# Optimization experiments

Measured on AMD Instinct MI355X. Metric: run time of the kernel, lower is better.

Reference implementation:

```python
import jax, jax.numpy as jnp
import numpy as np

N = 100_000      # nodes
E = 3_200_000    # edges (avg degree 32)
DIM = 512        # input feature dim
HID = 16         # GCNConv hidden dim (fixed in __init__)
C = 64           # n_classes
DROP_P = 0.5     # F.dropout default


def _gcn_conv(x, W, b, row, col, deg_inv_sqrt, n_nodes):
    """PyG GCNConv: h = x@W; out[j] += norm_ij * h[i]; out += b.
    row/col already include self-loops; deg_inv_sqrt precomputed."""
    h = x @ W                                  # [N, out]
    norm = deg_inv_sqrt[row] * deg_inv_sqrt[col]  # [E+N]
    msg = h[row] * norm[:, None]               # gather + scale
    out = jax.ops.segment_sum(msg, col, num_segments=n_nodes)
    return out + b


def setup_inputs() -> dict:
    key = jax.random.key(0)
    k = jax.random.split(key, 6)
    x = jax.random.normal(k[0], (N, DIM), dtype=jnp.float32)
    edge_index = jax.random.randint(k[1], (2, E), 0, N, dtype=jnp.int32)
    W1 = jax.random.normal(k[2], (DIM, HID), dtype=jnp.float32) * (1.0 / np.sqrt(DIM))
    b1 = jnp.zeros((HID,), dtype=jnp.float32)
    W2 = jax.random.normal(k[3], (HID, C), dtype=jnp.float32) * (1.0 / np.sqrt(HID))
    b2 = jnp.zeros((C,), dtype=jnp.float32)
    return {"x": x, "edge_index": edge_index, "W1": W1, "b1": b1, "W2": W2, "b2": b2}


def reference(x, edge_index, W1, b1, W2, b2):
    n = x.shape[0]
    loops = jnp.arange(n, dtype=edge_index.dtype)
    row = jnp.concatenate([edge_index[0], loops])  # sources (with self-loops)
    col = jnp.concatenate([edge_index[1], loops])  # targets (with self-loops)
    # symmetric normalization: deg over targets with unit edge weight
    deg = jax.ops.segment_sum(jnp.ones_like(col, dtype=x.dtype), col, num_segments=n)
    deg_inv_sqrt = jnp.where(deg > 0, jax.lax.rsqrt(deg), 0.0)

    h = jax.nn.relu(_gcn_conv(x, W1, b1, row, col, deg_inv_sqrt, n))
    # F.dropout(x) -> p=0.5, training=True; deterministic fixed key
    keep = jax.random.bernoulli(jax.random.key(42), 1.0 - DROP_P, h.shape)
    h = jnp.where(keep, h / (1.0 - DROP_P), 0.0)
    logits = _gcn_conv(h, W2, b2, row, col, deg_inv_sqrt, n)
    return jax.nn.log_softmax(logits, axis=1)
```

## Files before the change

kernel.cpp:

```cpp
#include <hip/hip_runtime.h>

#define NN    100000
#define NE    3200000
#define DIMK  512
#define HIDN  16
#define NCLS  64
#define NBUCK 391
#define NBLK  512
#define CHUNK 6250
#define BCAP  10240

__device__ __forceinline__ unsigned rotl32(unsigned x, int r){ return (x << r) | (x >> (32 - r)); }

__device__ __forceinline__ unsigned threefry_bits(unsigned i){
  const unsigned k0 = 0u, k1 = 42u;
  const unsigned k2 = 0x1BD11BDAu ^ k0 ^ k1;
  unsigned a = 0u + k0, b = i + k1;
#define TF_R(r) { a += b; b = rotl32(b, (r)); b ^= a; }
  TF_R(13) TF_R(15) TF_R(26) TF_R(6)  a += k1; b += k2 + 1u;
  TF_R(17) TF_R(29) TF_R(16) TF_R(24) a += k2; b += k0 + 2u;
  TF_R(13) TF_R(15) TF_R(26) TF_R(6)  a += k0; b += k1 + 3u;
  TF_R(17) TF_R(29) TF_R(16) TF_R(24) a += k1; b += k2 + 4u;
  TF_R(13) TF_R(15) TF_R(26) TF_R(6)  a += k2; b += k0 + 5u;
#undef TF_R
  return a ^ b;
}

__global__ __launch_bounds__(256) void kp1_hist(const int* __restrict__ col, int* __restrict__ M){
  __shared__ int h[NBUCK];
  const int blk = blockIdx.x, t = threadIdx.x;
  for (int q = t; q < NBUCK; q += 256) h[q] = 0;
  __syncthreads();
  const int e0 = blk * CHUNK;
  for (int i = t; i < CHUNK; i += 256)
    atomicAdd(&h[col[e0 + i] >> 8], 1);
  __syncthreads();
  for (int q = t; q < NBUCK; q += 256) M[blk * NBUCK + q] = h[q];
}

__global__ __launch_bounds__(512) void kp2_rowscan(int* __restrict__ M, int* __restrict__ btot){
  __shared__ int s[512];
  const int b = blockIdx.x, t = threadIdx.x;
  const int idx = t * NBUCK + b;
  int v = M[idx];
  int x = v;
  s[t] = x; __syncthreads();
  for (int d = 1; d < 512; d <<= 1){
    int y = (t >= d) ? s[t - d] : 0;
    __syncthreads();
    x += y; s[t] = x;
    __syncthreads();
  }
  M[idx] = x - v;
  if (t == 511) btot[b] = x;
}

__global__ __launch_bounds__(512) void kp2b_bscan(const int* __restrict__ btot, int* __restrict__ bbase){
  __shared__ int s[512];
  const int t = threadIdx.x;
  int v = (t < NBUCK) ? btot[t] : 0;
  int x = v;
  s[t] = x; __syncthreads();
  for (int d = 1; d < 512; d <<= 1){
    int y = (t >= d) ? s[t - d] : 0;
    __syncthreads();
    x += y; s[t] = x;
    __syncthreads();
  }
  if (t < NBUCK) bbase[t] = x - v;
  if (t == NBUCK - 1) bbase[NBUCK] = x;
}

__global__ __launch_bounds__(256) void kp3_scatter(const int* __restrict__ row, const int* __restrict__ col,
                                                   const int* __restrict__ M, const int* __restrict__ bbase,
                                                   unsigned* __restrict__ coarse){
  __shared__ int cur[NBUCK];
  const int blk = blockIdx.x, t = threadIdx.x;
  for (int q = t; q < NBUCK; q += 256) cur[q] = bbase[q] + M[blk * NBUCK + q];
  __syncthreads();
  const int e0 = blk * CHUNK;
  for (int i = t; i < CHUNK; i += 256){
    int c = col[e0 + i];
    int r = row[e0 + i];
    int p = atomicAdd(&cur[c >> 8], 1);
    coarse[p] = ((unsigned)(c & 255) << 17) | (unsigned)r;
  }
}

__global__ __launch_bounds__(1024) void kd_meta(const unsigned* __restrict__ coarse,
                                                const int* __restrict__ bbase,
                                                int* __restrict__ dstart,
                                                int* __restrict__ dcnt,
                                                float* __restrict__ dis){
  __shared__ int cnt[256], s[256];
  const int b = blockIdx.x, t = threadIdx.x;
  if (t < 256) cnt[t] = 0;
  __syncthreads();
  const int base = bbase[b];
  const int nreg = bbase[b + 1] - base;
  for (int i = t; i < nreg; i += 1024)
    atomicAdd(&cnt[coarse[base + i] >> 17], 1);
  __syncthreads();
  int deg = 0, x = 0;
  if (t < 256){ deg = cnt[t]; x = deg; s[t] = x; }
  __syncthreads();
  for (int d = 1; d < 256; d <<= 1){
    int y = 0;
    if (t < 256 && t >= d) y = s[t - d];
    __syncthreads();
    if (t < 256){ x += y; s[t] = x; }
    __syncthreads();
  }
  if (t < 256){
    int n = (b << 8) + t;
    if (n < NN){
      dstart[n] = base + (x - deg);
      dcnt[n]   = deg;
      dis[n]    = rsqrtf((float)(deg + 1));
    }
  }
}

__global__ __launch_bounds__(256) void k_gemm1(const float* __restrict__ x,
                                               const float* __restrict__ W1,
                                               const float* __restrict__ dis,
                                               _Float16* __restrict__ hs16){
  const int lane = threadIdx.x & 63;
  const int wid  = (blockIdx.x * blockDim.x + threadIdx.x) >> 6;
  const int nw   = (gridDim.x * blockDim.x) >> 6;
  const bool s5 = (lane & 32) != 0;
  const bool s4 = (lane & 16) != 0;
  const bool s3 = (lane & 8)  != 0;
  const bool s2 = (lane & 4)  != 0;

  float4 w4[8][4];
  const float4* W1v = (const float4*)W1;
#pragma unroll
  for (int k = 0; k < 8; ++k)
#pragma unroll
    for (int jj = 0; jj < 4; ++jj)
      w4[k][jj] = W1v[(lane * 8 + k) * 4 + jj];

  for (int n = wid; n < NN; n += nw){
    const float4* xp = (const float4*)(x + (size_t)n * DIMK + lane * 8);
    float4 xa = xp[0], xb = xp[1];
    float xv[8] = {xa.x, xa.y, xa.z, xa.w, xb.x, xb.y, xb.z, xb.w};
    float acc[16];
#pragma unroll
    for (int j = 0; j < 16; ++j) acc[j] = 0.f;
#pragma unroll
    for (int k = 0; k < 8; ++k){
      float xk = xv[k];
#pragma unroll
      for (int jj = 0; jj < 4; ++jj){
        acc[jj*4+0] = fmaf(xk, w4[k][jj].x, acc[jj*4+0]);
        acc[jj*4+1] = fmaf(xk, w4[k][jj].y, acc[jj*4+1]);
        acc[jj*4+2] = fmaf(xk, w4[k][jj].z, acc[jj*4+2]);
        acc[jj*4+3] = fmaf(xk, w4[k][jj].w, acc[jj*4+3]);
      }
    }
    float t8[8];
#pragma unroll
    for (int m = 0; m < 8; ++m){
      float keep = s5 ? acc[8+m] : acc[m];
      float give = s5 ? acc[m]   : acc[8+m];
      t8[m] = keep + __shfl_xor(give, 32, 64);
    }
    float t4[4];
#pragma unroll
    for (int m = 0; m < 4; ++m){
      float keep = s4 ? t8[4+m] : t8[m];
      float give = s4 ? t8[m]   : t8[4+m];
      t4[m] = keep + __shfl_xor(give, 16, 64);
    }
    float t2[2];
#pragma unroll
    for (int m = 0; m < 2; ++m){
      float keep = s3 ? t4[2+m] : t4[m];
      float give = s3 ? t4[m]   : t4[2+m];
      t2[m] = keep + __shfl_xor(give, 8, 64);
    }
    float keep = s2 ? t2[1] : t2[0];
    float give = s2 ? t2[0] : t2[1];
    float v = keep + __shfl_xor(give, 4, 64);
    v += __shfl_xor(v, 2, 64);
    v += __shfl_xor(v, 1, 64);
    float hv = __shfl(v, (lane & 15) * 4, 64);
    if (lane < 16) hs16[(size_t)n * HIDN + lane] = (_Float16)(hv * dis[n]);
  }
}

__global__ __launch_bounds__(1024) void k_sortagg1(const unsigned* __restrict__ coarse,
                                                   const int* __restrict__ bbase,
                                                   const int* __restrict__ dstart,
                                                   const int* __restrict__ dcnt,
                                                   const _Float16* __restrict__ hs16,
                                                   const float* __restrict__ dis,
                                                   const float* __restrict__ b1,
                                                   _Float16* __restrict__ h2s16){
  __shared__ int ldsCsr[BCAP];
  __shared__ int ofs[256], cnt[256], rk[256];
  const int b = blockIdx.x, t = threadIdx.x;
  const int base = bbase[b];
  const int nreg = min(bbase[b + 1] - base, BCAP);
  if (t < 256){
    int n = (b << 8) + t;
    rk[t] = 0;
    if (n < NN){ ofs[t] = dstart[n] - base; cnt[t] = dcnt[n]; }
    else       { ofs[t] = 0;               cnt[t] = 0; }
  }
  __syncthreads();
  for (int i = t; i < nreg; i += 1024){
    unsigned p = coarse[base + i];
    int l = p >> 17;
    int q = atomicAdd(&rk[l], 1);
    ldsCsr[ofs[l] + q] = (int)(p & 0x1FFFFu);
  }
  __syncthreads();
  const int g = t >> 4, j = t & 15;
  for (int d = g; d < 256; d += 64){
    const int n = (b << 8) + d;
    if (n >= NN) break;
    const int st = ofs[d], cn = cnt[d];
    float acc = 0.f;
    int i = 0;
    for (; i + 2 <= cn; i += 2){
      int r0 = ldsCsr[st + i];
      int r1 = ldsCsr[st + i + 1];
      float a0 = (float)hs16[r0 * HIDN + j];
      float a1 = (float)hs16[r1 * HIDN + j];
      acc += a0 + a1;
    }
    if (i < cn) acc += (float)hs16[ldsCsr[st + i] * HIDN + j];
    float dn = dis[n];
    float v = fmaf(dn, acc + (float)hs16[(size_t)n * HIDN + j], b1[j]);
    v = fmaxf(v, 0.f);
    unsigned bits = threefry_bits((unsigned)(n * HIDN + j));
    float kept = (bits & 0x80000000u) ? 0.f : v * 2.f;
    h2s16[(size_t)n * HIDN + j] = (_Float16)(kept * dn);
  }
}

__global__ __launch_bounds__(1024) void k_agg2b(const unsigned* __restrict__ coarse,
                                                const int* __restrict__ bbase,
                                                const int* __restrict__ dstart,
                                                const int* __restrict__ dcnt,
                                                const _Float16* __restrict__ h2s16,
                                                const float* __restrict__ dis,
                                                const float* __restrict__ W2,
                                                const float* __restrict__ b2,
                                                float* __restrict__ out){
  __shared__ int ldsCsr[BCAP];
  __shared__ int ofs[256], cnt[256], rk[256];
  __shared__ float accT[256 * HIDN];
  const int b = blockIdx.x, t = threadIdx.x;
  const int base = bbase[b];
  const int nreg = min(bbase[b + 1] - base, BCAP);
  if (t < 256){
    int n = (b << 8) + t;
    rk[t] = 0;
    if (n < NN){ ofs[t] = dstart[n] - base; cnt[t] = dcnt[n]; }
    else       { ofs[t] = 0;               cnt[t] = 0; }
  }
  __syncthreads();
  for (int i = t; i < nreg; i += 1024){
    unsigned p = coarse[base + i];
    int l = p >> 17;
    int q = atomicAdd(&rk[l], 1);
    ldsCsr[ofs[l] + q] = (int)(p & 0x1FFFFu);
  }
  __syncthreads();
  const int g = t >> 4, j = t & 15;
  for (int d = g; d < 256; d += 64){
    const int n = (b << 8) + d;
    float acc = 0.f;
    if (n < NN){
      const int st = ofs[d], cn = cnt[d];
      int i = 0;
      for (; i + 2 <= cn; i += 2){
        int r0 = ldsCsr[st + i];
        int r1 = ldsCsr[st + i + 1];
        acc += (float)h2s16[r0 * HIDN + j] + (float)h2s16[r1 * HIDN + j];
      }
      if (i < cn) acc += (float)h2s16[ldsCsr[st + i] * HIDN + j];
    }
    accT[d * HIDN + j] = acc;
  }
  __syncthreads();
  const int lane = t & 63, w = t >> 6;
  float wc[16];
#pragma unroll
  for (int k = 0; k < 16; ++k) wc[k] = W2[k * NCLS + lane];
  const float bb = b2[lane];
  for (int d = w; d < 256; d += 16){
    int n = (b << 8) + d;
    if (n >= NN) continue;
    float dn = dis[n];
    int jl = lane & 15;
    float aggj = dn * (accT[d * HIDN + jl] + (float)h2s16[(size_t)n * HIDN + jl]);
    float s = bb;
#pragma unroll
    for (int k = 0; k < 16; ++k) s = fmaf(__shfl(aggj, k, 64), wc[k], s);
    float m2 = s;
#pragma unroll
    for (int dd = 32; dd; dd >>= 1) m2 = fmaxf(m2, __shfl_xor(m2, dd, 64));
    float ex = __expf(s - m2);
    float sum = ex;
#pragma unroll
    for (int dd = 32; dd; dd >>= 1) sum += __shfl_xor(sum, dd, 64);
    out[(size_t)n * NCLS + lane] = (s - m2) - __logf(sum);
  }
}

extern "C" void kernel_launch(void* const* d_in, const int* in_sizes, int n_in,
                              void* d_out, int out_size, void* d_ws, size_t ws_size,
                              hipStream_t stream){
  const float* x  = (const float*)d_in[0];
  const int*   ei = (const int*)  d_in[1];
  const float* W1 = (const float*)d_in[2];
  const float* b1 = (const float*)d_in[3];
  const float* W2 = (const float*)d_in[4];
  const float* b2 = (const float*)d_in[5];
  float* out = (float*)d_out;
  const int* row = ei;
  const int* col = ei + NE;

  char* ws = (char*)d_ws;
  int*       M      = (int*)      (ws + 0);
  int*       btot   = (int*)      (ws + 800768);
  int*       bbase  = (int*)      (ws + 802368);
  int*       dstart = (int*)      (ws + 803968);
  int*       dcnt   = (int*)      (ws + 1203968);
  float*     dis    = (float*)    (ws + 1603968);
  unsigned*  coarse = (unsigned*) (ws + 2003968);
  _Float16*  hs16   = (_Float16*) (ws + 14803968);
  _Float16*  h2s16  = (_Float16*) (ws + 18003968);

  kp1_hist   <<<NBLK, 256, 0, stream>>>(col, M);
  kp2_rowscan<<<NBUCK, 512, 0, stream>>>(M, btot);
  kp2b_bscan <<<1, 512, 0, stream>>>(btot, bbase);
  kp3_scatter<<<NBLK, 256, 0, stream>>>(row, col, M, bbase, coarse);
  kd_meta    <<<NBUCK, 1024, 0, stream>>>(coarse, bbase, dstart, dcnt, dis);
  k_gemm1    <<<1024, 256, 0, stream>>>(x, W1, dis, hs16);
  k_sortagg1 <<<NBUCK, 1024, 0, stream>>>(coarse, bbase, dstart, dcnt, hs16, dis, b1, h2s16);
  k_agg2b    <<<NBUCK, 1024, 0, stream>>>(coarse, bbase, dstart, dcnt, h2s16, dis, W2, b2, out);
}
```

Measured before the change: 507.6 us.

## Fuse histogram with GEMM1 launch, compute degree via global atomics, drop kd_meta

The edge histogram blocks and the x@W1 projection now run in one launch, so the bandwidth-heavy GEMM overlaps with the histogram. Node degrees come from global atomics in the histogram pass, and dis is computed in the row scan, which removes the kd_meta kernel. The per-node counts and offsets are rebuilt in LDS inside both aggregation kernels. Because h1 is no longer prescaled by dis, layer 1 gathers dis[r] per edge, and both gather loops unroll to 4. This trades an extra memset, 3.2M global atomics, a redundant in-block count and scan, and extra per-edge gathers for one fewer launch and GEMM/histogram overlap.

```diff
diff --git a/kernel.cpp b/kernel.cpp
--- a/kernel.cpp
+++ b/kernel.cpp
@@ -26,19 +26,95 @@
   return a ^ b;
 }
 
-__global__ __launch_bounds__(256) void kp1_hist(const int* __restrict__ col, int* __restrict__ M){
+__global__ __launch_bounds__(256) void k_front(const float* __restrict__ x,
+                                               const float* __restrict__ W1,
+                                               const int* __restrict__ col,
+                                               int* __restrict__ M,
+                                               int* __restrict__ dcnt0,
+                                               _Float16* __restrict__ h1){
   __shared__ int h[NBUCK];
-  const int blk = blockIdx.x, t = threadIdx.x;
-  for (int q = t; q < NBUCK; q += 256) h[q] = 0;
-  __syncthreads();
-  const int e0 = blk * CHUNK;
-  for (int i = t; i < CHUNK; i += 256)
-    atomicAdd(&h[col[e0 + i] >> 8], 1);
-  __syncthreads();
-  for (int q = t; q < NBUCK; q += 256) M[blk * NBUCK + q] = h[q];
-}
-
-__global__ __launch_bounds__(512) void kp2_rowscan(int* __restrict__ M, int* __restrict__ btot){
+  if (blockIdx.x < NBLK){
+    const int blk = blockIdx.x, t = threadIdx.x;
+    for (int q = t; q < NBUCK; q += 256) h[q] = 0;
+    __syncthreads();
+    const int e0 = blk * CHUNK;
+    for (int i = t; i < CHUNK; i += 256){
+      int c = col[e0 + i];
+      atomicAdd(&h[c >> 8], 1);
+      atomicAdd(&dcnt0[c], 1);
+    }
+    __syncthreads();
+    for (int q = t; q < NBUCK; q += 256) M[blk * NBUCK + q] = h[q];
+    return;
+  }
+  const int lane = threadIdx.x & 63;
+  const int wid  = (blockIdx.x - NBLK) * 4 + (threadIdx.x >> 6);
+  const int nw   = 1024 * 4;
+  const bool s5 = (lane & 32) != 0;
+  const bool s4 = (lane & 16) != 0;
+  const bool s3 = (lane & 8)  != 0;
+  const bool s2 = (lane & 4)  != 0;
+
+  float4 w4[8][4];
+  const float4* W1v = (const float4*)W1;
+#pragma unroll
+  for (int k = 0; k < 8; ++k)
+#pragma unroll
+    for (int jj = 0; jj < 4; ++jj)
+      w4[k][jj] = W1v[(lane * 8 + k) * 4 + jj];
+
+  for (int n = wid; n < NN; n += nw){
+    const float4* xp = (const float4*)(x + (size_t)n * DIMK + lane * 8);
+    float4 xa = xp[0], xb = xp[1];
+    float xv[8] = {xa.x, xa.y, xa.z, xa.w, xb.x, xb.y, xb.z, xb.w};
+    float acc[16];
+#pragma unroll
+    for (int j = 0; j < 16; ++j) acc[j] = 0.f;
+#pragma unroll
+    for (int k = 0; k < 8; ++k){
+      float xk = xv[k];
+#pragma unroll
+      for (int jj = 0; jj < 4; ++jj){
+        acc[jj*4+0] = fmaf(xk, w4[k][jj].x, acc[jj*4+0]);
+        acc[jj*4+1] = fmaf(xk, w4[k][jj].y, acc[jj*4+1]);
+        acc[jj*4+2] = fmaf(xk, w4[k][jj].z, acc[jj*4+2]);
+        acc[jj*4+3] = fmaf(xk, w4[k][jj].w, acc[jj*4+3]);
+      }
+    }
+    float t8[8];
+#pragma unroll
+    for (int m = 0; m < 8; ++m){
+      float keep = s5 ? acc[8+m] : acc[m];
+      float give = s5 ? acc[m]   : acc[8+m];
+      t8[m] = keep + __shfl_xor(give, 32, 64);
+    }
+    float t4[4];
+#pragma unroll
+    for (int m = 0; m < 4; ++m){
+      float keep = s4 ? t8[4+m] : t8[m];
+      float give = s4 ? t8[m]   : t8[4+m];
+      t4[m] = keep + __shfl_xor(give, 16, 64);
+    }
+    float t2[2];
+#pragma unroll
+    for (int m = 0; m < 2; ++m){
+      float keep = s3 ? t4[2+m] : t4[m];
+      float give = s3 ? t4[m]   : t4[2+m];
+      t2[m] = keep + __shfl_xor(give, 8, 64);
+    }
+    float keep = s2 ? t2[1] : t2[0];
+    float give = s2 ? t2[0] : t2[1];
+    float v = keep + __shfl_xor(give, 4, 64);
+    v += __shfl_xor(v, 2, 64);
+    v += __shfl_xor(v, 1, 64);
+    float hv = __shfl(v, (lane & 15) * 4, 64);
+    if (lane < 16) h1[(size_t)n * HIDN + lane] = (_Float16)hv;
+  }
+}
+
+__global__ __launch_bounds__(512) void kp2_rowscan(int* __restrict__ M, int* __restrict__ btot,
+                                                   const int* __restrict__ dcnt0,
+                                                   float* __restrict__ dis){
   __shared__ int s[512];
   const int b = blockIdx.x, t = threadIdx.x;
   const int idx = t * NBUCK + b;
@@ -53,6 +129,10 @@
   }
   M[idx] = x - v;
   if (t == 511) btot[b] = x;
+  if (t < 256){
+    int n = (b << 8) + t;
+    if (n < NN) dis[n] = rsqrtf((float)(dcnt0[n] + 1));
+  }
 }
 
 __global__ __launch_bounds__(512) void kp2b_bscan(const int* __restrict__ btot, int* __restrict__ bbase){
@@ -87,128 +167,33 @@
   }
 }
 
-__global__ __launch_bounds__(1024) void kd_meta(const unsigned* __restrict__ coarse,
-                                                const int* __restrict__ bbase,
-                                                int* __restrict__ dstart,
-                                                int* __restrict__ dcnt,
-                                                float* __restrict__ dis){
-  __shared__ int cnt[256], s[256];
-  const int b = blockIdx.x, t = threadIdx.x;
-  if (t < 256) cnt[t] = 0;
-  __syncthreads();
-  const int base = bbase[b];
-  const int nreg = bbase[b + 1] - base;
-  for (int i = t; i < nreg; i += 1024)
-    atomicAdd(&cnt[coarse[base + i] >> 17], 1);
-  __syncthreads();
-  int deg = 0, x = 0;
-  if (t < 256){ deg = cnt[t]; x = deg; s[t] = x; }
-  __syncthreads();
-  for (int d = 1; d < 256; d <<= 1){
-    int y = 0;
-    if (t < 256 && t >= d) y = s[t - d];
-    __syncthreads();
-    if (t < 256){ x += y; s[t] = x; }
-    __syncthreads();
-  }
-  if (t < 256){
-    int n = (b << 8) + t;
-    if (n < NN){
-      dstart[n] = base + (x - deg);
-      dcnt[n]   = deg;
-      dis[n]    = rsqrtf((float)(deg + 1));
-    }
-  }
-}
-
-__global__ __launch_bounds__(256) void k_gemm1(const float* __restrict__ x,
-                                               const float* __restrict__ W1,
-                                               const float* __restrict__ dis,
-                                               _Float16* __restrict__ hs16){
-  const int lane = threadIdx.x & 63;
-  const int wid  = (blockIdx.x * blockDim.x + threadIdx.x) >> 6;
-  const int nw   = (gridDim.x * blockDim.x) >> 6;
-  const bool s5 = (lane & 32) != 0;
-  const bool s4 = (lane & 16) != 0;
-  const bool s3 = (lane & 8)  != 0;
-  const bool s2 = (lane & 4)  != 0;
-
-  float4 w4[8][4];
-  const float4* W1v = (const float4*)W1;
-#pragma unroll
-  for (int k = 0; k < 8; ++k)
-#pragma unroll
-    for (int jj = 0; jj < 4; ++jj)
-      w4[k][jj] = W1v[(lane * 8 + k) * 4 + jj];
-
-  for (int n = wid; n < NN; n += nw){
-    const float4* xp = (const float4*)(x + (size_t)n * DIMK + lane * 8);
-    float4 xa = xp[0], xb = xp[1];
-    float xv[8] = {xa.x, xa.y, xa.z, xa.w, xb.x, xb.y, xb.z, xb.w};
-    float acc[16];
-#pragma unroll
-    for (int j = 0; j < 16; ++j) acc[j] = 0.f;
-#pragma unroll
-    for (int k = 0; k < 8; ++k){
-      float xk = xv[k];
-#pragma unroll
-      for (int jj = 0; jj < 4; ++jj){
-        acc[jj*4+0] = fmaf(xk, w4[k][jj].x, acc[jj*4+0]);
-        acc[jj*4+1] = fmaf(xk, w4[k][jj].y, acc[jj*4+1]);
-        acc[jj*4+2] = fmaf(xk, w4[k][jj].z, acc[jj*4+2]);
-        acc[jj*4+3] = fmaf(xk, w4[k][jj].w, acc[jj*4+3]);
-      }
-    }
-    float t8[8];
-#pragma unroll
-    for (int m = 0; m < 8; ++m){
-      float keep = s5 ? acc[8+m] : acc[m];
-      float give = s5 ? acc[m]   : acc[8+m];
-      t8[m] = keep + __shfl_xor(give, 32, 64);
-    }
-    float t4[4];
-#pragma unroll
-    for (int m = 0; m < 4; ++m){
-      float keep = s4 ? t8[4+m] : t8[m];
-      float give = s4 ? t8[m]   : t8[4+m];
-      t4[m] = keep + __shfl_xor(give, 16, 64);
-    }
-    float t2[2];
-#pragma unroll
-    for (int m = 0; m < 2; ++m){
-      float keep = s3 ? t4[2+m] : t4[m];
-      float give = s3 ? t4[m]   : t4[2+m];
-      t2[m] = keep + __shfl_xor(give, 8, 64);
-    }
-    float keep = s2 ? t2[1] : t2[0];
-    float give = s2 ? t2[0] : t2[1];
-    float v = keep + __shfl_xor(give, 4, 64);
-    v += __shfl_xor(v, 2, 64);
-    v += __shfl_xor(v, 1, 64);
-    float hv = __shfl(v, (lane & 15) * 4, 64);
-    if (lane < 16) hs16[(size_t)n * HIDN + lane] = (_Float16)(hv * dis[n]);
-  }
-}
-
 __global__ __launch_bounds__(1024) void k_sortagg1(const unsigned* __restrict__ coarse,
                                                    const int* __restrict__ bbase,
-                                                   const int* __restrict__ dstart,
-                                                   const int* __restrict__ dcnt,
-                                                   const _Float16* __restrict__ hs16,
+                                                   const _Float16* __restrict__ h1,
                                                    const float* __restrict__ dis,
                                                    const float* __restrict__ b1,
                                                    _Float16* __restrict__ h2s16){
   __shared__ int ldsCsr[BCAP];
-  __shared__ int ofs[256], cnt[256], rk[256];
+  __shared__ int cnt[256], ofs[256], rk[256], s[256];
   const int b = blockIdx.x, t = threadIdx.x;
   const int base = bbase[b];
   const int nreg = min(bbase[b + 1] - base, BCAP);
-  if (t < 256){
-    int n = (b << 8) + t;
-    rk[t] = 0;
-    if (n < NN){ ofs[t] = dstart[n] - base; cnt[t] = dcnt[n]; }
-    else       { ofs[t] = 0;               cnt[t] = 0; }
-  }
+  if (t < 256){ cnt[t] = 0; rk[t] = 0; }
+  __syncthreads();
+  for (int i = t; i < nreg; i += 1024)
+    atomicAdd(&cnt[coarse[base + i] >> 17], 1);
+  __syncthreads();
+  int deg = 0, x = 0;
+  if (t < 256){ deg = cnt[t]; x = deg; s[t] = x; }
+  __syncthreads();
+  for (int d = 1; d < 256; d <<= 1){
+    int y = 0;
+    if (t < 256 && t >= d) y = s[t - d];
+    __syncthreads();
+    if (t < 256){ x += y; s[t] = x; }
+    __syncthreads();
+  }
+  if (t < 256) ofs[t] = x - deg;
   __syncthreads();
   for (int i = t; i < nreg; i += 1024){
     unsigned p = coarse[base + i];
@@ -224,16 +209,20 @@
     const int st = ofs[d], cn = cnt[d];
     float acc = 0.f;
     int i = 0;
-    for (; i + 2 <= cn; i += 2){
+    for (; i + 4 <= cn; i += 4){
+      int r0 = ldsCsr[st + i],     r1 = ldsCsr[st + i + 1];
+      int r2 = ldsCsr[st + i + 2], r3 = ldsCsr[st + i + 3];
+      float d0 = dis[r0], d1 = dis[r1], d2 = dis[r2], d3 = dis[r3];
+      float a0 = (float)h1[r0 * HIDN + j], a1 = (float)h1[r1 * HIDN + j];
+      float a2 = (float)h1[r2 * HIDN + j], a3 = (float)h1[r3 * HIDN + j];
+      acc += d0 * a0 + d1 * a1 + d2 * a2 + d3 * a3;
+    }
+    for (; i < cn; ++i){
       int r0 = ldsCsr[st + i];
-      int r1 = ldsCsr[st + i + 1];
-      float a0 = (float)hs16[r0 * HIDN + j];
-      float a1 = (float)hs16[r1 * HIDN + j];
-      acc += a0 + a1;
-    }
-    if (i < cn) acc += (float)hs16[ldsCsr[st + i] * HIDN + j];
+      acc += dis[r0] * (float)h1[r0 * HIDN + j];
+    }
     float dn = dis[n];
-    float v = fmaf(dn, acc + (float)hs16[(size_t)n * HIDN + j], b1[j]);
+    float v = fmaf(dn, acc + dn * (float)h1[(size_t)n * HIDN + j], b1[j]);
     v = fmaxf(v, 0.f);
     unsigned bits = threefry_bits((unsigned)(n * HIDN + j));
     float kept = (bits & 0x80000000u) ? 0.f : v * 2.f;
@@ -243,25 +232,33 @@
 
 __global__ __launch_bounds__(1024) void k_agg2b(const unsigned* __restrict__ coarse,
                                                 const int* __restrict__ bbase,
-                                                const int* __restrict__ dstart,
-                                                const int* __restrict__ dcnt,
                                                 const _Float16* __restrict__ h2s16,
                                                 const float* __restrict__ dis,
                                                 const float* __restrict__ W2,
                                                 const float* __restrict__ b2,
                                                 float* __restrict__ out){
   __shared__ int ldsCsr[BCAP];
-  __shared__ int ofs[256], cnt[256], rk[256];
+  __shared__ int cnt[256], ofs[256], rk[256], s[256];
   __shared__ float accT[256 * HIDN];
   const int b = blockIdx.x, t = threadIdx.x;
   const int base = bbase[b];
   const int nreg = min(bbase[b + 1] - base, BCAP);
-  if (t < 256){
-    int n = (b << 8) + t;
-    rk[t] = 0;
-    if (n < NN){ ofs[t] = dstart[n] - base; cnt[t] = dcnt[n]; }
-    else       { ofs[t] = 0;               cnt[t] = 0; }
-  }
+  if (t < 256){ cnt[t] = 0; rk[t] = 0; }
+  __syncthreads();
+  for (int i = t; i < nreg; i += 1024)
+    atomicAdd(&cnt[coarse[base + i] >> 17], 1);
+  __syncthreads();
+  int deg = 0, x = 0;
+  if (t < 256){ deg = cnt[t]; x = deg; s[t] = x; }
+  __syncthreads();
+  for (int d = 1; d < 256; d <<= 1){
+    int y = 0;
+    if (t < 256 && t >= d) y = s[t - d];
+    __syncthreads();
+    if (t < 256){ x += y; s[t] = x; }
+    __syncthreads();
+  }
+  if (t < 256) ofs[t] = x - deg;
   __syncthreads();
   for (int i = t; i < nreg; i += 1024){
     unsigned p = coarse[base + i];
@@ -277,12 +274,13 @@
     if (n < NN){
       const int st = ofs[d], cn = cnt[d];
       int i = 0;
-      for (; i + 2 <= cn; i += 2){
-        int r0 = ldsCsr[st + i];
-        int r1 = ldsCsr[st + i + 1];
-        acc += (float)h2s16[r0 * HIDN + j] + (float)h2s16[r1 * HIDN + j];
+      for (; i + 4 <= cn; i += 4){
+        int r0 = ldsCsr[st + i],     r1 = ldsCsr[st + i + 1];
+        int r2 = ldsCsr[st + i + 2], r3 = ldsCsr[st + i + 3];
+        acc += (float)h2s16[r0 * HIDN + j] + (float)h2s16[r1 * HIDN + j]
+             + (float)h2s16[r2 * HIDN + j] + (float)h2s16[r3 * HIDN + j];
       }
-      if (i < cn) acc += (float)h2s16[ldsCsr[st + i] * HIDN + j];
+      for (; i < cn; ++i) acc += (float)h2s16[ldsCsr[st + i] * HIDN + j];
     }
     accT[d * HIDN + j] = acc;
   }
@@ -298,17 +296,17 @@
     float dn = dis[n];
     int jl = lane & 15;
     float aggj = dn * (accT[d * HIDN + jl] + (float)h2s16[(size_t)n * HIDN + jl]);
-    float s = bb;
-#pragma unroll
-    for (int k = 0; k < 16; ++k) s = fmaf(__shfl(aggj, k, 64), wc[k], s);
-    float m2 = s;
+    float s2v = bb;
+#pragma unroll
+    for (int k = 0; k < 16; ++k) s2v = fmaf(__shfl(aggj, k, 64), wc[k], s2v);
+    float m2 = s2v;
 #pragma unroll
     for (int dd = 32; dd; dd >>= 1) m2 = fmaxf(m2, __shfl_xor(m2, dd, 64));
-    float ex = __expf(s - m2);
+    float ex = __expf(s2v - m2);
     float sum = ex;
 #pragma unroll
     for (int dd = 32; dd; dd >>= 1) sum += __shfl_xor(sum, dd, 64);
-    out[(size_t)n * NCLS + lane] = (s - m2) - __logf(sum);
+    out[(size_t)n * NCLS + lane] = (s2v - m2) - __logf(sum);
   }
 }
 
@@ -329,19 +327,17 @@
   int*       M      = (int*)      (ws + 0);
   int*       btot   = (int*)      (ws + 800768);
   int*       bbase  = (int*)      (ws + 802368);
-  int*       dstart = (int*)      (ws + 803968);
-  int*       dcnt   = (int*)      (ws + 1203968);
-  float*     dis    = (float*)    (ws + 1603968);
-  unsigned*  coarse = (unsigned*) (ws + 2003968);
-  _Float16*  hs16   = (_Float16*) (ws + 14803968);
-  _Float16*  h2s16  = (_Float16*) (ws + 18003968);
-
-  kp1_hist   <<<NBLK, 256, 0, stream>>>(col, M);
-  kp2_rowscan<<<NBUCK, 512, 0, stream>>>(M, btot);
+  int*       dcnt0  = (int*)      (ws + 803968);
+  float*     dis    = (float*)    (ws + 1203968);
+  unsigned*  coarse = (unsigned*) (ws + 1603968);
+  _Float16*  h1     = (_Float16*) (ws + 14403968);
+  _Float16*  h2s16  = (_Float16*) (ws + 17603968);
+
+  hipMemsetAsync(dcnt0, 0, NN * sizeof(int), stream);
+  k_front    <<<NBLK + 1024, 256, 0, stream>>>(x, W1, col, M, dcnt0, h1);
+  kp2_rowscan<<<NBUCK, 512, 0, stream>>>(M, btot, dcnt0, dis);
   kp2b_bscan <<<1, 512, 0, stream>>>(btot, bbase);
   kp3_scatter<<<NBLK, 256, 0, stream>>>(row, col, M, bbase, coarse);
-  kd_meta    <<<NBUCK, 1024, 0, stream>>>(coarse, bbase, dstart, dcnt, dis);
-  k_gemm1    <<<1024, 256, 0, stream>>>(x, W1, dis, hs16);
-  k_sortagg1 <<<NBUCK, 1024, 0, stream>>>(coarse, bbase, dstart, dcnt, hs16, dis, b1, h2s16);
-  k_agg2b    <<<NBUCK, 1024, 0, stream>>>(coarse, bbase, dstart, dcnt, h2s16, dis, W2, b2, out);
-}
+  k_sortagg1 <<<NBUCK, 1024, 0, stream>>>(coarse, bbase, h1, dis, b1, h2s16);
+  k_agg2b    <<<NBUCK, 1024, 0, stream>>>(coarse, bbase, h2s16, dis, W2, b2, out);
+}
```

Measured after the change: 589.5 us. 1.16x slower.
